# Performance work log

Measured on AMD Instinct MI355X. Metric: run time of the kernel, lower is better.

The kernel has to match this reference:

```python
import jax, jax.numpy as jnp
import numpy as np

B, S, D, H = 2, 2048, 1024, 16
HD = D // H  # 64


def setup_inputs() -> dict:
    key = jax.random.key(0)
    ks = jax.random.split(key, 7)
    s = 1.0 / np.sqrt(HD)
    return {
        "x": jax.random.normal(ks[0], (B, S, D), dtype=jnp.float32),
        "Wq": jax.random.normal(ks[1], (H, HD, HD), dtype=jnp.float32) * s,
        "bq": jax.random.normal(ks[2], (H, HD), dtype=jnp.float32) * 0.01,
        "Wk": jax.random.normal(ks[3], (H, HD, HD), dtype=jnp.float32) * s,
        "bk": jax.random.normal(ks[4], (H, HD), dtype=jnp.float32) * 0.01,
        "Wv": jax.random.normal(ks[5], (H, HD, HD), dtype=jnp.float32) * s,
        "bv": jax.random.normal(ks[6], (H, HD), dtype=jnp.float32) * 0.01,
    }


def reference(x, Wq, bq, Wk, bk, Wv, bv):
    b, s, d = x.shape
    h, hd, _ = Wq.shape
    # Faithful to torch: x.view(B, H, S, hd) is a raw reshape (mixes seq positions
    # across heads), NOT a transpose-based head split.
    xh = x.reshape(b, h, s, hd)
    # torch Linear: y @ W.T + b, with W of shape (out, in)
    q = jnp.einsum('bhse,hde->bhsd', xh, Wq) + bq[None, :, None, :]
    k = jnp.einsum('bhse,hde->bhsd', xh, Wk) + bk[None, :, None, :]
    v = jnp.einsum('bhse,hde->bhsd', xh, Wv) + bv[None, :, None, :]
    scale = 1.0 / jnp.sqrt(jnp.asarray(d / h, dtype=jnp.float32))
    attn = jax.nn.softmax(jnp.einsum('bhqd,bhkd->bhqk', q, k) * scale, axis=-1)
    out = jnp.einsum('bhqk,bhkd->bhqd', attn, v)
    # torch.cat over heads along last dim == transpose then merge
    return out.transpose(0, 2, 1, 3).reshape(b, s, d)
```

## Files before the change

kernel.cpp:

```cpp
#include <hip/hip_runtime.h>
#include <hip/hip_bf16.h>

#define BATCH 2
#define SEQ   2048
#define DMODEL 1024
#define NH    16
#define HD    64
#define QSCALE 0.1803368801111602f

typedef __attribute__((ext_vector_type(8))) short bf16x8;
typedef __attribute__((ext_vector_type(4))) float f32x4;

__device__ __forceinline__ ushort f2bf(float f) {
    union { float f; unsigned u; } v; v.f = f;
    return (ushort)((v.u + 0x8000u) >> 16);
}

__device__ __forceinline__ unsigned pack2bf(float a, float b) {
    union { float f; unsigned u; } x, y; x.f = a; y.f = b;
    return __builtin_amdgcn_perm(y.u + 0x8000u, x.u + 0x8000u, 0x07060302u);
}

__device__ __forceinline__ float exp2r(float x) {
#if __has_builtin(__builtin_amdgcn_exp2f)
    return __builtin_amdgcn_exp2f(x);
#else
    return exp2f(x);
#endif
}

__device__ __forceinline__ void g2l16(const void* g, void* l) {
    __builtin_amdgcn_global_load_lds(
        (const __attribute__((address_space(1))) unsigned*)g,
        (__attribute__((address_space(3))) unsigned*)l, 16, 0, 0);
}

#define MFMA(a, b, c) __builtin_amdgcn_mfma_f32_16x16x32_bf16((a), (b), (c), 0, 0, 0)

__global__ __launch_bounds__(256) void wfmt_kernel(
    const float* __restrict__ Wq, const float* __restrict__ Wk,
    const float* __restrict__ Wv, ushort* __restrict__ Wf)
{
    const int blk = blockIdx.x;
    const int h = blk / 3, m = blk - h * 3;
    const float* W = (m == 0 ? Wq : (m == 1 ? Wk : Wv)) + h * 4096;
    const float s = (m == 0) ? QSCALE : 1.0f;
    for (int i = 0; i < 2; ++i) {
        int idx = threadIdx.x + 256 * i;
        int l = idx & 63, chunk = idx >> 6;
        int qd = l >> 4, l16 = l & 15, nt = chunk >> 1, ks = chunk & 1;
        const float* src = W + (nt * 16 + l16) * 64 + ks * 32 + qd * 8;
        float4 a = *(const float4*)src;
        float4 b = *(const float4*)(src + 4);
        union { bf16x8 v; unsigned u[4]; } t;
        t.u[0] = pack2bf(a.x * s, a.y * s);
        t.u[1] = pack2bf(a.z * s, a.w * s);
        t.u[2] = pack2bf(b.x * s, b.y * s);
        t.u[3] = pack2bf(b.z * s, b.w * s);
        *(bf16x8*)&Wf[((size_t)blk * 512 + idx) * 8] = t.v;
    }
}

__global__ __launch_bounds__(256) void qkv_kernel(
    const float* __restrict__ x, const ushort* __restrict__ Wf,
    const float* __restrict__ bq, const float* __restrict__ bk,
    const float* __restrict__ bv,
    ushort* __restrict__ Qo, ushort* __restrict__ Kf, ushort* __restrict__ Vf)
{
    const int bid = blockIdx.x;
    const int st  = bid & 31;
    const int bh  = bid >> 5;
    const int h   = bh & (NH - 1);

    __shared__ ushort EbQ[64 * 72];
    __shared__ ushort EbK[64 * 72];
    __shared__ ushort EbV[64 * 72];

    const int tid  = threadIdx.x;
    const int wave = tid >> 6, lane = tid & 63;
    const int ln16 = lane & 15, quad = lane >> 4;

    const float* xr = x + (size_t)bh * (SEQ * HD)
                        + ((size_t)st * 64 + wave * 16 + ln16) * HD;
    bf16x8 afr[2];
#pragma unroll
    for (int ks = 0; ks < 2; ++ks) {
        const float4* p = (const float4*)(xr + ks * 32 + quad * 8);
        float4 a = p[0], b = p[1];
        union { bf16x8 v; unsigned u[4]; } t;
        t.u[0] = pack2bf(a.x, a.y);
        t.u[1] = pack2bf(a.z, a.w);
        t.u[2] = pack2bf(b.x, b.y);
        t.u[3] = pack2bf(b.z, b.w);
        afr[ks] = t.v;
    }

    const bf16x8* wf = (const bf16x8*)Wf + (size_t)h * 1536 + lane;

    f32x4 acc[3][4];
#pragma unroll
    for (int m = 0; m < 3; ++m)
#pragma unroll
        for (int nt = 0; nt < 4; ++nt) {
            f32x4 a = {0.f, 0.f, 0.f, 0.f};
            a = MFMA(afr[0], wf[(m * 8 + nt * 2 + 0) * 64], a);
            a = MFMA(afr[1], wf[(m * 8 + nt * 2 + 1) * 64], a);
            acc[m][nt] = a;
        }

#pragma unroll
    for (int nt = 0; nt < 4; ++nt) {
        float bbq = bq[h * 64 + nt * 16 + ln16] * QSCALE;
        float bbk = bk[h * 64 + nt * 16 + ln16];
#pragma unroll
        for (int r = 0; r < 4; ++r) {
            EbQ[(wave * 16 + quad * 4 + r) * 72 + nt * 16 + ln16] = f2bf(acc[0][nt][r] + bbq);
            EbK[(wave * 16 + quad * 4 + r) * 72 + nt * 16 + ln16] = f2bf(acc[1][nt][r] + bbk);
        }
        float bbv = bv[h * 64 + nt * 16 + ln16];
        ushort4 o;
        o.x = f2bf(acc[2][nt][0] + bbv);
        o.y = f2bf(acc[2][nt][1] + bbv);
        o.z = f2bf(acc[2][nt][2] + bbv);
        o.w = f2bf(acc[2][nt][3] + bbv);
        *(ushort4*)&EbV[(nt * 16 + ln16) * 72 + wave * 16 + quad * 4] = o;
    }
    __syncthreads();

    {
        ushort* dst = Qo + (size_t)bh * SEQ * HD + (size_t)st * 64 * HD;
        for (int i = 0; i < 2; ++i) {
            int idx = tid + 256 * i;
            int row = idx >> 3, c8 = (idx & 7) * 8;
            *(bf16x8*)&dst[row * 64 + c8] = *(const bf16x8*)&EbQ[row * 72 + c8];
        }
    }
    {
        ushort* dstK = Kf + ((size_t)bh * 32 + st) * 4096;
        ushort* dstV = Vf + ((size_t)bh * 32 + st) * 4096;
        for (int i = 0; i < 2; ++i) {
            int idx8 = tid + 256 * i;
            int l2 = idx8 & 63, chunk = idx8 >> 6;
            int nt = chunk >> 1, ks = chunk & 1;
            int qd = l2 >> 4, l16 = l2 & 15;
            *(bf16x8*)&dstK[(size_t)idx8 * 8] =
                *(const bf16x8*)&EbK[(nt * 16 + l16) * 72 + ks * 32 + qd * 8];
            *(bf16x8*)&dstV[(size_t)idx8 * 8] =
                *(const bf16x8*)&EbV[(nt * 16 + l16) * 72 + ks * 32 + qd * 8];
        }
    }
}

__global__ __launch_bounds__(256, 2) void attn_kernel(
    const ushort* __restrict__ Q, const ushort* __restrict__ Kf,
    const ushort* __restrict__ Vf, float* __restrict__ out)
{
    const int bid = blockIdx.x;
    const int wid = (bid & 7) * 64 + (bid >> 3);
    const int qt  = wid & 15;
    const int bh  = wid >> 4;
    const int h   = bh & (NH - 1), b = bh >> 4;

    __shared__ ushort Ksh[3][4096];
    __shared__ ushort Vsh[3][4096];
    __shared__ ushort Ps[4][2][2048];

    const int tid = threadIdx.x, wave = tid >> 6, lane = tid & 63;
    const int ln16 = lane & 15, quad = lane >> 4;
    const unsigned swz = (unsigned)(ln16 & 7) << 4;

    const char* kgb = (const char*)Kf + (size_t)bh * 32 * 8192 + wave * 2048 + lane * 16;
    const char* vgb = (const char*)Vf + (size_t)bh * 32 * 8192 + wave * 2048 + lane * 16;

    auto stage = [&](int kt, int sb) {
        const char* kg = kgb + (size_t)kt * 8192;
        const char* vg = vgb + (size_t)kt * 8192;
        ushort* kl = &Ksh[sb][wave * 1024];
        ushort* vl = &Vsh[sb][wave * 1024];
        g2l16(kg,        kl);
        g2l16(kg + 1024, kl + 512);
        g2l16(vg,        vl);
        g2l16(vg + 1024, vl + 512);
    };

    stage(0, 0);
    stage(1, 1);

    bf16x8 qfr[2][2];
#pragma unroll
    for (int g = 0; g < 2; ++g) {
        const ushort* Qg = Q + ((size_t)bh * SEQ + qt * 128 + wave * 32 + g * 16 + ln16) * HD;
        qfr[g][0] = *(const bf16x8*)&Qg[quad * 8];
        qfr[g][1] = *(const bf16x8*)&Qg[32 + quad * 8];
    }

    float lsum[2] = {0.f, 0.f};
    f32x4 accO[2][4];
#pragma unroll
    for (int g = 0; g < 2; ++g)
#pragma unroll
        for (int nt = 0; nt < 4; ++nt) accO[g][nt] = (f32x4){0.f, 0.f, 0.f, 0.f};

    bf16x8 vf[8];

    for (int kt = 0; kt < 32; ++kt) {
        const int cur = kt & 1;
        const int sb  = kt % 3;

        if (kt < 31) {
            asm volatile("s_waitcnt vmcnt(4)" ::: "memory");
        } else {
            asm volatile("s_waitcnt vmcnt(0)" ::: "memory");
        }
        __builtin_amdgcn_s_barrier();
        __builtin_amdgcn_sched_barrier(0);

        const ushort* Kb = &Ksh[sb][0];
        bf16x8 kf[8];
#pragma unroll
        for (int c = 0; c < 8; ++c) kf[c] = *(const bf16x8*)&Kb[c * 512 + lane * 8];

        f32x4 sacc[2][4];
        __builtin_amdgcn_s_setprio(1);
#pragma unroll
        for (int nt = 0; nt < 4; ++nt)
#pragma unroll
            for (int g = 0; g < 2; ++g) {
                f32x4 a = {0.f, 0.f, 0.f, 0.f};
                a = MFMA(kf[nt * 2],     qfr[g][0], a);
                a = MFMA(kf[nt * 2 + 1], qfr[g][1], a);
                sacc[g][nt] = a;
            }
        __builtin_amdgcn_s_setprio(0);

        if (kt > 0) {
            const char* Pr = (const char*)Ps[wave][1 - cur];
            bf16x8 pf[2][2];
#pragma unroll
            for (int g = 0; g < 2; ++g) {
                const char* Prr = Pr + (g * 16 + ln16) * 128;
                pf[g][0] = *(const bf16x8*)(Prr + (((unsigned)(quad * 16)) ^ swz));
                pf[g][1] = *(const bf16x8*)(Prr + (((unsigned)(64 + quad * 16)) ^ swz));
            }
            __builtin_amdgcn_s_setprio(1);
#pragma unroll
            for (int nt = 0; nt < 4; ++nt)
#pragma unroll
                for (int g = 0; g < 2; ++g) {
                    accO[g][nt] = MFMA(vf[nt * 2],     pf[g][0], accO[g][nt]);
                    accO[g][nt] = MFMA(vf[nt * 2 + 1], pf[g][1], accO[g][nt]);
                }
            __builtin_amdgcn_s_setprio(0);
        }

        const ushort* Vb = &Vsh[sb][0];
#pragma unroll
        for (int c = 0; c < 8; ++c) vf[c] = *(const bf16x8*)&Vb[c * 512 + lane * 8];

        char* Pw = (char*)Ps[wave][cur];
#pragma unroll
        for (int g = 0; g < 2; ++g) {
            char* Pwr = Pw + (g * 16 + ln16) * 128;
            float rs = 0.f;
#pragma unroll
            for (int nt = 0; nt < 4; ++nt) {
                float p0 = exp2r(sacc[g][nt][0]);
                float p1 = exp2r(sacc[g][nt][1]);
                float p2 = exp2r(sacc[g][nt][2]);
                float p3 = exp2r(sacc[g][nt][3]);
                rs += (p0 + p1) + (p2 + p3);
                uint2 pk;
                pk.x = pack2bf(p0, p1);
                pk.y = pack2bf(p2, p3);
                *(uint2*)(Pwr + (((unsigned)(nt * 32 + quad * 8)) ^ swz)) = pk;
            }
            lsum[g] += rs;
        }

        if (kt < 30) {
            asm volatile("s_waitcnt lgkmcnt(0)" ::: "memory");
            __builtin_amdgcn_sched_barrier(0);
            stage(kt + 2, (kt + 2) % 3);
        }
    }

    {
        const char* Pr = (const char*)Ps[wave][1];
        bf16x8 pf[2][2];
#pragma unroll
        for (int g = 0; g < 2; ++g) {
            const char* Prr = Pr + (g * 16 + ln16) * 128;
            pf[g][0] = *(const bf16x8*)(Prr + (((unsigned)(quad * 16)) ^ swz));
            pf[g][1] = *(const bf16x8*)(Prr + (((unsigned)(64 + quad * 16)) ^ swz));
        }
#pragma unroll
        for (int nt = 0; nt < 4; ++nt)
#pragma unroll
            for (int g = 0; g < 2; ++g) {
                accO[g][nt] = MFMA(vf[nt * 2],     pf[g][0], accO[g][nt]);
                accO[g][nt] = MFMA(vf[nt * 2 + 1], pf[g][1], accO[g][nt]);
            }
    }

#pragma unroll
    for (int g = 0; g < 2; ++g) {
        float l = lsum[g];
        l += __shfl_xor(l, 16, 64);
        l += __shfl_xor(l, 32, 64);
        float rinv = 1.0f / l;
        float* ob = out + ((size_t)b * SEQ + qt * 128 + wave * 32 + g * 16 + ln16) * DMODEL + h * HD;
#pragma unroll
        for (int nt = 0; nt < 4; ++nt) {
            float4 o;
            o.x = accO[g][nt][0] * rinv;
            o.y = accO[g][nt][1] * rinv;
            o.z = accO[g][nt][2] * rinv;
            o.w = accO[g][nt][3] * rinv;
            *(float4*)&ob[nt * 16 + quad * 4] = o;
        }
    }
}

extern "C" void kernel_launch(void* const* d_in, const int* in_sizes, int n_in,
                              void* d_out, int out_size, void* d_ws, size_t ws_size,
                              hipStream_t stream) {
    const float* x  = (const float*)d_in[0];
    const float* Wq = (const float*)d_in[1];
    const float* bq = (const float*)d_in[2];
    const float* Wk = (const float*)d_in[3];
    const float* bk = (const float*)d_in[4];
    const float* Wv = (const float*)d_in[5];
    const float* bv = (const float*)d_in[6];

    const size_t nElem = (size_t)BATCH * NH * SEQ * HD;
    ushort* Qw  = (ushort*)d_ws;
    ushort* Kw  = Qw + nElem;
    ushort* Vw  = Kw + nElem;
    ushort* Wfw = Vw + nElem;

    wfmt_kernel<<<48, 256, 0, stream>>>(Wq, Wk, Wv, Wfw);
    qkv_kernel<<<32 * 32, 256, 0, stream>>>(
        x, Wfw, bq, bk, bv, Qw, Kw, Vw);
    attn_kernel<<<BATCH * NH * (SEQ / 128), 256, 0, stream>>>(
        Qw, Kw, Vw, (float*)d_out);
}
```

Baseline: 132.5 us.

## Fuse weight formatting into QKV kernel and simplify attention to direct K/V loads

```diff
diff --git a/kernel.cpp b/kernel.cpp
--- a/kernel.cpp
+++ b/kernel.cpp
@@ -29,42 +29,13 @@
 #endif
 }
 
-__device__ __forceinline__ void g2l16(const void* g, void* l) {
-    __builtin_amdgcn_global_load_lds(
-        (const __attribute__((address_space(1))) unsigned*)g,
-        (__attribute__((address_space(3))) unsigned*)l, 16, 0, 0);
-}
-
 #define MFMA(a, b, c) __builtin_amdgcn_mfma_f32_16x16x32_bf16((a), (b), (c), 0, 0, 0)
 
-__global__ __launch_bounds__(256) void wfmt_kernel(
-    const float* __restrict__ Wq, const float* __restrict__ Wk,
-    const float* __restrict__ Wv, ushort* __restrict__ Wf)
-{
-    const int blk = blockIdx.x;
-    const int h = blk / 3, m = blk - h * 3;
-    const float* W = (m == 0 ? Wq : (m == 1 ? Wk : Wv)) + h * 4096;
-    const float s = (m == 0) ? QSCALE : 1.0f;
-    for (int i = 0; i < 2; ++i) {
-        int idx = threadIdx.x + 256 * i;
-        int l = idx & 63, chunk = idx >> 6;
-        int qd = l >> 4, l16 = l & 15, nt = chunk >> 1, ks = chunk & 1;
-        const float* src = W + (nt * 16 + l16) * 64 + ks * 32 + qd * 8;
-        float4 a = *(const float4*)src;
-        float4 b = *(const float4*)(src + 4);
-        union { bf16x8 v; unsigned u[4]; } t;
-        t.u[0] = pack2bf(a.x * s, a.y * s);
-        t.u[1] = pack2bf(a.z * s, a.w * s);
-        t.u[2] = pack2bf(b.x * s, b.y * s);
-        t.u[3] = pack2bf(b.z * s, b.w * s);
-        *(bf16x8*)&Wf[((size_t)blk * 512 + idx) * 8] = t.v;
-    }
-}
-
 __global__ __launch_bounds__(256) void qkv_kernel(
-    const float* __restrict__ x, const ushort* __restrict__ Wf,
-    const float* __restrict__ bq, const float* __restrict__ bk,
-    const float* __restrict__ bv,
+    const float* __restrict__ x,
+    const float* __restrict__ Wq, const float* __restrict__ bq,
+    const float* __restrict__ Wk, const float* __restrict__ bk,
+    const float* __restrict__ Wv, const float* __restrict__ bv,
     ushort* __restrict__ Qo, ushort* __restrict__ Kf, ushort* __restrict__ Vf)
 {
     const int bid = blockIdx.x;
@@ -95,18 +66,34 @@
         afr[ks] = t.v;
     }
 
-    const bf16x8* wf = (const bf16x8*)Wf + (size_t)h * 1536 + lane;
+    const float* wsrc[3] = { Wq + h * 4096, Wk + h * 4096, Wv + h * 4096 };
 
     f32x4 acc[3][4];
 #pragma unroll
-    for (int m = 0; m < 3; ++m)
+    for (int m = 0; m < 3; ++m) {
+        const float s = (m == 0) ? QSCALE : 1.0f;
+        bf16x8 bfr[8];
+#pragma unroll
+        for (int j = 0; j < 8; ++j) {
+            int nt = j >> 1, ks = j & 1;
+            const float* src = wsrc[m] + (nt * 16 + ln16) * 64 + ks * 32 + quad * 8;
+            float4 a = *(const float4*)src;
+            float4 b = *(const float4*)(src + 4);
+            union { bf16x8 v; unsigned u[4]; } t;
+            t.u[0] = pack2bf(a.x * s, a.y * s);
+            t.u[1] = pack2bf(a.z * s, a.w * s);
+            t.u[2] = pack2bf(b.x * s, b.y * s);
+            t.u[3] = pack2bf(b.z * s, b.w * s);
+            bfr[j] = t.v;
+        }
 #pragma unroll
         for (int nt = 0; nt < 4; ++nt) {
             f32x4 a = {0.f, 0.f, 0.f, 0.f};
-            a = MFMA(afr[0], wf[(m * 8 + nt * 2 + 0) * 64], a);
-            a = MFMA(afr[1], wf[(m * 8 + nt * 2 + 1) * 64], a);
+            a = MFMA(afr[0], bfr[nt * 2 + 0], a);
+            a = MFMA(afr[1], bfr[nt * 2 + 1], a);
             acc[m][nt] = a;
         }
+    }
 
 #pragma unroll
     for (int nt = 0; nt < 4; ++nt) {
@@ -151,164 +138,120 @@
     }
 }
 
-__global__ __launch_bounds__(256, 2) void attn_kernel(
+__global__ __launch_bounds__(256) void attn_kernel(
     const ushort* __restrict__ Q, const ushort* __restrict__ Kf,
     const ushort* __restrict__ Vf, float* __restrict__ out)
 {
     const int bid = blockIdx.x;
-    const int wid = (bid & 7) * 64 + (bid >> 3);
-    const int qt  = wid & 15;
-    const int bh  = wid >> 4;
+    const int wid = (bid & 7) * 32 + (bid >> 3);
+    const int qt  = wid & 7;
+    const int bh  = wid >> 3;
     const int h   = bh & (NH - 1), b = bh >> 4;
 
-    __shared__ ushort Ksh[3][4096];
-    __shared__ ushort Vsh[3][4096];
-    __shared__ ushort Ps[4][2][2048];
+    __shared__ ushort Ps[4][2][64 * 72];
 
     const int tid = threadIdx.x, wave = tid >> 6, lane = tid & 63;
     const int ln16 = lane & 15, quad = lane >> 4;
-    const unsigned swz = (unsigned)(ln16 & 7) << 4;
-
-    const char* kgb = (const char*)Kf + (size_t)bh * 32 * 8192 + wave * 2048 + lane * 16;
-    const char* vgb = (const char*)Vf + (size_t)bh * 32 * 8192 + wave * 2048 + lane * 16;
-
-    auto stage = [&](int kt, int sb) {
-        const char* kg = kgb + (size_t)kt * 8192;
-        const char* vg = vgb + (size_t)kt * 8192;
-        ushort* kl = &Ksh[sb][wave * 1024];
-        ushort* vl = &Vsh[sb][wave * 1024];
-        g2l16(kg,        kl);
-        g2l16(kg + 1024, kl + 512);
-        g2l16(vg,        vl);
-        g2l16(vg + 1024, vl + 512);
-    };
-
-    stage(0, 0);
-    stage(1, 1);
-
-    bf16x8 qfr[2][2];
-#pragma unroll
-    for (int g = 0; g < 2; ++g) {
-        const ushort* Qg = Q + ((size_t)bh * SEQ + qt * 128 + wave * 32 + g * 16 + ln16) * HD;
+
+    bf16x8 qfr[4][2];
+#pragma unroll
+    for (int g = 0; g < 4; ++g) {
+        const ushort* Qg = Q + ((size_t)bh * SEQ + qt * 256 + wave * 64 + g * 16 + ln16) * HD;
         qfr[g][0] = *(const bf16x8*)&Qg[quad * 8];
         qfr[g][1] = *(const bf16x8*)&Qg[32 + quad * 8];
     }
 
-    float lsum[2] = {0.f, 0.f};
-    f32x4 accO[2][4];
-#pragma unroll
-    for (int g = 0; g < 2; ++g)
+    const bf16x8* kfp = (const bf16x8*)(Kf + (size_t)bh * 32 * 4096) + lane;
+    const bf16x8* vfp = (const bf16x8*)(Vf + (size_t)bh * 32 * 4096) + lane;
+
+    float lsum[4] = {0.f, 0.f, 0.f, 0.f};
+    f32x4 accO[4][4];
+#pragma unroll
+    for (int g = 0; g < 4; ++g)
 #pragma unroll
         for (int nt = 0; nt < 4; ++nt) accO[g][nt] = (f32x4){0.f, 0.f, 0.f, 0.f};
-
-    bf16x8 vf[8];
 
     for (int kt = 0; kt < 32; ++kt) {
         const int cur = kt & 1;
-        const int sb  = kt % 3;
-
-        if (kt < 31) {
-            asm volatile("s_waitcnt vmcnt(4)" ::: "memory");
-        } else {
-            asm volatile("s_waitcnt vmcnt(0)" ::: "memory");
-        }
-        __builtin_amdgcn_s_barrier();
-        __builtin_amdgcn_sched_barrier(0);
-
-        const ushort* Kb = &Ksh[sb][0];
+
         bf16x8 kf[8];
 #pragma unroll
-        for (int c = 0; c < 8; ++c) kf[c] = *(const bf16x8*)&Kb[c * 512 + lane * 8];
-
-        f32x4 sacc[2][4];
-        __builtin_amdgcn_s_setprio(1);
-#pragma unroll
-        for (int nt = 0; nt < 4; ++nt)
-#pragma unroll
-            for (int g = 0; g < 2; ++g) {
+        for (int c = 0; c < 8; ++c) kf[c] = kfp[c * 64];
+        kfp += 512;
+
+        bf16x8 vf[8];
+        if (kt > 0) {
+#pragma unroll
+            for (int c = 0; c < 8; ++c) vf[c] = vfp[c * 64];
+        }
+
+        const ushort* Pr = Ps[wave][1 - cur];
+        ushort* Pw = Ps[wave][cur];
+
+#pragma unroll
+        for (int g = 0; g < 4; ++g) {
+            f32x4 sacc[4];
+#pragma unroll
+            for (int nt = 0; nt < 4; ++nt) {
                 f32x4 a = {0.f, 0.f, 0.f, 0.f};
                 a = MFMA(kf[nt * 2],     qfr[g][0], a);
                 a = MFMA(kf[nt * 2 + 1], qfr[g][1], a);
-                sacc[g][nt] = a;
-            }
-        __builtin_amdgcn_s_setprio(0);
-
-        if (kt > 0) {
-            const char* Pr = (const char*)Ps[wave][1 - cur];
-            bf16x8 pf[2][2];
-#pragma unroll
-            for (int g = 0; g < 2; ++g) {
-                const char* Prr = Pr + (g * 16 + ln16) * 128;
-                pf[g][0] = *(const bf16x8*)(Prr + (((unsigned)(quad * 16)) ^ swz));
-                pf[g][1] = *(const bf16x8*)(Prr + (((unsigned)(64 + quad * 16)) ^ swz));
-            }
-            __builtin_amdgcn_s_setprio(1);
-#pragma unroll
-            for (int nt = 0; nt < 4; ++nt)
-#pragma unroll
-                for (int g = 0; g < 2; ++g) {
-                    accO[g][nt] = MFMA(vf[nt * 2],     pf[g][0], accO[g][nt]);
-                    accO[g][nt] = MFMA(vf[nt * 2 + 1], pf[g][1], accO[g][nt]);
+                sacc[nt] = a;
+            }
+
+            if (kt > 0) {
+                bf16x8 pf0 = *(const bf16x8*)&Pr[(g * 16 + ln16) * 72 + quad * 8];
+                bf16x8 pf1 = *(const bf16x8*)&Pr[(g * 16 + ln16) * 72 + 32 + quad * 8];
+#pragma unroll
+                for (int nt = 0; nt < 4; ++nt) {
+                    accO[g][nt] = MFMA(vf[nt * 2],     pf0, accO[g][nt]);
+                    accO[g][nt] = MFMA(vf[nt * 2 + 1], pf1, accO[g][nt]);
                 }
-            __builtin_amdgcn_s_setprio(0);
-        }
-
-        const ushort* Vb = &Vsh[sb][0];
-#pragma unroll
-        for (int c = 0; c < 8; ++c) vf[c] = *(const bf16x8*)&Vb[c * 512 + lane * 8];
-
-        char* Pw = (char*)Ps[wave][cur];
-#pragma unroll
-        for (int g = 0; g < 2; ++g) {
-            char* Pwr = Pw + (g * 16 + ln16) * 128;
+            }
+
             float rs = 0.f;
 #pragma unroll
             for (int nt = 0; nt < 4; ++nt) {
-                float p0 = exp2r(sacc[g][nt][0]);
-                float p1 = exp2r(sacc[g][nt][1]);
-                float p2 = exp2r(sacc[g][nt][2]);
-                float p3 = exp2r(sacc[g][nt][3]);
+                float p0 = exp2r(sacc[nt][0]);
+                float p1 = exp2r(sacc[nt][1]);
+                float p2 = exp2r(sacc[nt][2]);
+                float p3 = exp2r(sacc[nt][3]);
                 rs += (p0 + p1) + (p2 + p3);
                 uint2 pk;
                 pk.x = pack2bf(p0, p1);
                 pk.y = pack2bf(p2, p3);
-                *(uint2*)(Pwr + (((unsigned)(nt * 32 + quad * 8)) ^ swz)) = pk;
+                *(uint2*)&Pw[(g * 16 + ln16) * 72 + nt * 16 + quad * 4] = pk;
             }
             lsum[g] += rs;
         }
 
-        if (kt < 30) {
-            asm volatile("s_waitcnt lgkmcnt(0)" ::: "memory");
-            __builtin_amdgcn_sched_barrier(0);
-            stage(kt + 2, (kt + 2) % 3);
-        }
+        if (kt > 0) vfp += 512;
     }
 
     {
-        const char* Pr = (const char*)Ps[wave][1];
-        bf16x8 pf[2][2];
-#pragma unroll
-        for (int g = 0; g < 2; ++g) {
-            const char* Prr = Pr + (g * 16 + ln16) * 128;
-            pf[g][0] = *(const bf16x8*)(Prr + (((unsigned)(quad * 16)) ^ swz));
-            pf[g][1] = *(const bf16x8*)(Prr + (((unsigned)(64 + quad * 16)) ^ swz));
-        }
-#pragma unroll
-        for (int nt = 0; nt < 4; ++nt)
-#pragma unroll
-            for (int g = 0; g < 2; ++g) {
-                accO[g][nt] = MFMA(vf[nt * 2],     pf[g][0], accO[g][nt]);
-                accO[g][nt] = MFMA(vf[nt * 2 + 1], pf[g][1], accO[g][nt]);
-            }
-    }
-
-#pragma unroll
-    for (int g = 0; g < 2; ++g) {
+        bf16x8 vf[8];
+#pragma unroll
+        for (int c = 0; c < 8; ++c) vf[c] = vfp[c * 64];
+        const ushort* Pr = Ps[wave][1];
+#pragma unroll
+        for (int g = 0; g < 4; ++g) {
+            bf16x8 pf0 = *(const bf16x8*)&Pr[(g * 16 + ln16) * 72 + quad * 8];
+            bf16x8 pf1 = *(const bf16x8*)&Pr[(g * 16 + ln16) * 72 + 32 + quad * 8];
+#pragma unroll
+            for (int nt = 0; nt < 4; ++nt) {
+                accO[g][nt] = MFMA(vf[nt * 2],     pf0, accO[g][nt]);
+                accO[g][nt] = MFMA(vf[nt * 2 + 1], pf1, accO[g][nt]);
+            }
+        }
+    }
+
+#pragma unroll
+    for (int g = 0; g < 4; ++g) {
         float l = lsum[g];
         l += __shfl_xor(l, 16, 64);
         l += __shfl_xor(l, 32, 64);
         float rinv = 1.0f / l;
-        float* ob = out + ((size_t)b * SEQ + qt * 128 + wave * 32 + g * 16 + ln16) * DMODEL + h * HD;
+        float* ob = out + ((size_t)b * SEQ + qt * 256 + wave * 64 + g * 16 + ln16) * DMODEL + h * HD;
 #pragma unroll
         for (int nt = 0; nt < 4; ++nt) {
             float4 o;
@@ -333,14 +276,12 @@
     const float* bv = (const float*)d_in[6];
 
     const size_t nElem = (size_t)BATCH * NH * SEQ * HD;
-    ushort* Qw  = (ushort*)d_ws;
-    ushort* Kw  = Qw + nElem;
-    ushort* Vw  = Kw + nElem;
-    ushort* Wfw = Vw + nElem;
-
-    wfmt_kernel<<<48, 256, 0, stream>>>(Wq, Wk, Wv, Wfw);
+    ushort* Qw = (ushort*)d_ws;
+    ushort* Kw = Qw + nElem;
+    ushort* Vw = Kw + nElem;
+
     qkv_kernel<<<32 * 32, 256, 0, stream>>>(
-        x, Wfw, bq, bk, bv, Qw, Kw, Vw);
-    attn_kernel<<<BATCH * NH * (SEQ / 128), 256, 0, stream>>>(
+        x, Wq, bq, Wk, bk, Wv, bv, Qw, Kw, Vw);
+    attn_kernel<<<BATCH * NH * (SEQ / 128 / 2), 256, 0, stream>>>(
         Qw, Kw, Vw, (float*)d_out);
 }
```

Measured after the change: 168.2 us. +27.0%, slower.
